# Performance work log

Hardware: AMD Instinct MI355X
Metric: run time of the kernel (lower is better)

Reference implementation:

```python
import jax, jax.numpy as jnp
import numpy as np

LN_EPS = 1e-5
NORM_EPS = 1e-12  # F.normalize eps


def _l2norm(x):
    # torch F.normalize(p=2, dim=-1): x / max(||x||, eps)
    n = jnp.sqrt(jnp.sum(x * x, axis=-1, keepdims=True))
    return x / jnp.maximum(n, NORM_EPS)


def setup_inputs() -> dict:
    key = jax.random.key(0)
    D, R, H = 256, 32, 64  # d_model, rank, d_model//4
    B, C, P = 32, 64, 96
    ks = jax.random.split(key, 16)
    s = 0.05
    return {
        "x": jax.random.normal(ks[0], (B * C, P, D), jnp.float32),
        "ln_gamma": jnp.ones((D,), jnp.float32),
        "ln_beta": jnp.zeros((D,), jnp.float32),
        "Wd": jax.random.normal(ks[1], (D, R), jnp.float32) * s,
        "bd": jax.random.normal(ks[2], (R,), jnp.float32) * s,
        "Wq": jax.random.normal(ks[3], (R, R), jnp.float32) * s,
        "Wk": jax.random.normal(ks[4], (R, R), jnp.float32) * s,
        "Wv": jax.random.normal(ks[5], (R, R), jnp.float32) * s,
        "Wg": jax.random.normal(ks[6], (R, R), jnp.float32) * s,
        "bg": jax.random.normal(ks[7], (R,), jnp.float32) * s,
        "Wu": jax.random.normal(ks[8], (R, D), jnp.float32) * s,
        "bu": jax.random.normal(ks[9], (D,), jnp.float32) * s,
        "W1": jax.random.normal(ks[10], (D, H), jnp.float32) * s,
        "b1": jax.random.normal(ks[11], (H,), jnp.float32) * s,
        "W2": jax.random.normal(ks[12], (H, D), jnp.float32) * s,
        "b2": jnp.full((D,), -5.0, jnp.float32),  # gate_init bias
        "B": B,
        "C": C,
    }


def reference(x, ln_gamma, ln_beta, Wd, bd, Wq, Wk, Wv, Wg, bg, Wu, bu, W1, b1, W2, b2, B, C):
    BC, P, D = x.shape
    # [B*C, P, D] -> [B*P, C, D] channel-mixing layout
    h = x.reshape(B, C, P, D).transpose(0, 2, 1, 3).reshape(B * P, C, D)

    # LayerNorm over D (biased variance, as in torch LayerNorm)
    mu = jnp.mean(h, axis=-1, keepdims=True)
    var = jnp.var(h, axis=-1, keepdims=True)
    h_norm = (h - mu) * jax.lax.rsqrt(var + LN_EPS) * ln_gamma + ln_beta

    # bottleneck projection to rank R
    h_low = h_norm @ Wd + bd  # [BP, C, R]

    # Hydra linear attention: cosine-normalized Q/K, sum-pooled K*V global feature
    Q = _l2norm(h_low @ Wq)
    K = _l2norm(h_low @ Wk)
    V = h_low @ Wv
    global_feat = jnp.sum(K * V, axis=1, keepdims=True)  # [BP, 1, R]
    h_attn = Q * global_feat

    # content gate and up-projection
    gate_c = jax.nn.sigmoid(h_low @ Wg + bg)
    mixed = (h_attn * gate_c) @ Wu + bu  # [BP, C, D]

    # AdaptiveGate: unbiased variance over channel dim (torch .var default ddof=1)
    chan_var = jnp.var(h, axis=1, ddof=1)  # [BP, D]
    gate_logits = jax.nn.gelu(chan_var @ W1 + b1, approximate=False) @ W2 + b2
    gate = jax.nn.sigmoid(gate_logits)[:, None, :]  # [BP, 1, D]

    out = h + gate * mixed
    # back to [B*C, P, D]
    return out.reshape(B, P, C, D).transpose(0, 2, 1, 3).reshape(BC, P, D)
```

## Files before the change

### kernel.cpp

```cpp
#include <hip/hip_runtime.h>

#define DD 256
#define RR 32
#define CC 64
#define PB 96
#define NT 1024

typedef __attribute__((ext_vector_type(8))) short short8;
typedef __attribute__((ext_vector_type(4))) float f32x4;

__device__ __forceinline__ unsigned short f2b(float f) {
    union { float f; unsigned u; } v; v.f = f;
    unsigned r = v.u + 0x7fffu + ((v.u >> 16) & 1u);
    return (unsigned short)(r >> 16);
}
__device__ __forceinline__ float b2f(unsigned short s) {
    union { unsigned u; float f; } v; v.u = ((unsigned)s) << 16;
    return v.f;
}

__device__ __forceinline__ int hidx(int c, int d) {
    return c * 256 + ((((d >> 3) ^ (c & 7)) << 3) | (d & 7));
}
__device__ __forceinline__ int nidx(int row, int k) {
    return row * 32 + ((((k >> 3) ^ ((row >> 1) & 3)) << 3) | (k & 7));
}

__global__ __launch_bounds__(NT, 8)
void hydra_kernel(const float* __restrict__ x,
                  const float* __restrict__ ln_g, const float* __restrict__ ln_b,
                  const float* __restrict__ Wd, const float* __restrict__ bd,
                  const float* __restrict__ Wq, const float* __restrict__ Wk,
                  const float* __restrict__ Wv, const float* __restrict__ Wg,
                  const float* __restrict__ bg,
                  const float* __restrict__ Wu, const float* __restrict__ bu,
                  const float* __restrict__ W1, const float* __restrict__ b1,
                  const float* __restrict__ W2, const float* __restrict__ b2,
                  float* __restrict__ out)
{
    __shared__ short hbf[CC * DD];
    __shared__ short wreg[RR * DD];
    __shared__ short lowbuf[CC * RR];
    __shared__ short qgkv[2 * CC * RR];
    __shared__ float redA[2048];
    __shared__ float redB[1024];
    __shared__ float mu_s[CC], rstd_s[CC];
    __shared__ float cv_s[DD], gate_s[DD];
    __shared__ float hid_s[64];
    __shared__ float ln_a[RR], ln_bv[RR];

    const int t    = threadIdx.x;
    const int lane = t & 63;
    const int w    = t >> 6;
    const int bp   = blockIdx.x;
    const int b    = bp / PB;
    const int p    = bp - b * PB;
    const size_t rowbase = (size_t)(b * CC) * PB * DD + (size_t)p * DD;

    #pragma unroll
    for (int i = 0; i < 4; ++i) {
        const int c = w * 4 + i;
        const float4 v = *(const float4*)(x + rowbase + (size_t)c * (PB * DD) + 4 * lane);
        float s1 = v.x + v.y + v.z + v.w;
        float s2 = v.x * v.x + v.y * v.y + v.z * v.z + v.w * v.w;
        #pragma unroll
        for (int off = 32; off; off >>= 1) {
            s1 += __shfl_xor(s1, off, 64);
            s2 += __shfl_xor(s2, off, 64);
        }
        if (lane == 0) {
            const float mu = s1 * (1.f / 256.f);
            mu_s[c]   = mu;
            rstd_s[c] = rsqrtf(s2 * (1.f / 256.f) - mu * mu + 1e-5f);
        }
        ushort4 pk;
        pk.x = f2b(v.x); pk.y = f2b(v.y); pk.z = f2b(v.z); pk.w = f2b(v.w);
        *(ushort4*)&hbf[hidx(c, 4 * lane)] = pk;
    }
    {
        const int r = t >> 5, dblk = t & 31;
        short8 vv;
        float sa = 0.f, sb = 0.f;
        #pragma unroll
        for (int j = 0; j < 8; ++j) {
            const int d = dblk * 8 + j;
            const float wd = Wd[d * RR + r];
            const float g  = ln_g[d];
            vv[j] = (short)f2b(g * wd);
            sa += g * wd;
            sb += ln_b[d] * wd;
        }
        *(short8*)&wreg[r * 256 + ((dblk ^ (r & 7)) << 3)] = vv;
        redA[r * 32 + dblk]        = sa;
        redA[1024 + r * 32 + dblk] = sb;
    }
    __syncthreads();

    f32x4 s3acc = {0.f, 0.f, 0.f, 0.f};
    if (w < 8) {
        const int ct = w >> 1, rt = w & 1;
        const int arow = ct * 16 + (lane & 15);
        const int brow = rt * 16 + (lane & 15);
        const int ksub = lane >> 4;
        #pragma unroll
        for (int step = 0; step < 8; ++step) {
            const int kb = step * 4 + ksub;
            const short8 a  = *(const short8*)&hbf[arow * 256 + ((kb ^ (arow & 7)) << 3)];
            const short8 bf = *(const short8*)&wreg[brow * 256 + ((kb ^ (brow & 7)) << 3)];
            s3acc = __builtin_amdgcn_mfma_f32_16x16x32_bf16(a, bf, s3acc, 0, 0, 0);
        }
    } else {
        const int idx = t - 512;
        const int d = idx & 255, half = idx >> 8;
        float s1 = 0.f, s2 = 0.f;
        #pragma unroll 8
        for (int i = 0; i < 32; ++i) {
            const float v = b2f((unsigned short)hbf[hidx(half * 32 + i, d)]);
            s1 += v; s2 += v * v;
        }
        redB[half * 256 + d]       = s1;
        redB[512 + half * 256 + d] = s2;
        if (idx < 64) {
            const int r = idx & 31, which = idx >> 5;
            float s = 0.f;
            for (int g = 0; g < 32; ++g) s += redA[which * 1024 + r * 32 + g];
            if (which == 0) ln_a[r] = s;
            else            ln_bv[r] = s + bd[r];
        }
    }
    __syncthreads();

    if (w < 8) {
        const int ct = w >> 1, rt = w & 1;
        const int col = rt * 16 + (lane & 15);
        const float la = ln_a[col], lb = ln_bv[col];
        #pragma unroll
        for (int i = 0; i < 4; ++i) {
            const int c = ct * 16 + (lane >> 4) * 4 + i;
            const float rs = rstd_s[c];
            const float hl = rs * s3acc[i] - rs * mu_s[c] * la + lb;
            lowbuf[nidx(c, col)] = (short)f2b(hl);
        }
    } else {
        const int slot = t - 512;
        const int m = slot >> 7, rr2 = (slot >> 2) & 31, kg = slot & 3;
        const float* Wm = (m == 0) ? Wq : (m == 1) ? Wk : (m == 2) ? Wv : Wg;
        short8 vv;
        #pragma unroll
        for (int j = 0; j < 8; ++j)
            vv[j] = (short)f2b(Wm[(kg * 8 + j) * RR + rr2]);
        *(short8*)&wreg[m * 1024 + nidx(rr2, kg * 8)] = vv;
    }
    if (t < 256) {
        const float S1 = redB[t] + redB[256 + t];
        const float S2 = redB[512 + t] + redB[768 + t];
        cv_s[t] = (S2 - S1 * S1 * (1.f / 64.f)) * (1.f / 63.f);
    }
    __syncthreads();

    if (w < 8) {
        const int ct = w >> 1, pair = w & 1;
        const int mA = pair ? 1 : 0;
        const int mB = pair ? 2 : 3;
        const int arow = ct * 16 + (lane & 15);
        const int ksub = lane >> 4;
        const short8 a = *(const short8*)&lowbuf[arow * 32 + ((ksub ^ ((arow >> 1) & 3)) << 3)];
        f32x4 aA0 = {0,0,0,0}, aA1 = {0,0,0,0}, aB0 = {0,0,0,0}, aB1 = {0,0,0,0};
        {
            const int br0 = (lane & 15), br1 = 16 + (lane & 15);
            const short8 bA0 = *(const short8*)&wreg[mA * 1024 + br0 * 32 + ((ksub ^ ((br0 >> 1) & 3)) << 3)];
            const short8 bA1 = *(const short8*)&wreg[mA * 1024 + br1 * 32 + ((ksub ^ ((br1 >> 1) & 3)) << 3)];
            const short8 bB0 = *(const short8*)&wreg[mB * 1024 + br0 * 32 + ((ksub ^ ((br0 >> 1) & 3)) << 3)];
            const short8 bB1 = *(const short8*)&wreg[mB * 1024 + br1 * 32 + ((ksub ^ ((br1 >> 1) & 3)) << 3)];
            aA0 = __builtin_amdgcn_mfma_f32_16x16x32_bf16(a, bA0, aA0, 0, 0, 0);
            aA1 = __builtin_amdgcn_mfma_f32_16x16x32_bf16(a, bA1, aA1, 0, 0, 0);
            aB0 = __builtin_amdgcn_mfma_f32_16x16x32_bf16(a, bB0, aB0, 0, 0, 0);
            aB1 = __builtin_amdgcn_mfma_f32_16x16x32_bf16(a, bB1, aB1, 0, 0, 0);
        }
        float qs[4];
        #pragma unroll
        for (int i = 0; i < 4; ++i) {
            float ss = aA0[i] * aA0[i] + aA1[i] * aA1[i];
            ss += __shfl_xor(ss, 1, 64);
            ss += __shfl_xor(ss, 2, 64);
            ss += __shfl_xor(ss, 4, 64);
            ss += __shfl_xor(ss, 8, 64);
            qs[i] = 1.f / fmaxf(sqrtf(ss), 1e-12f);
        }
        const int col0 = (lane & 15), col1 = 16 + (lane & 15);
        float bgv0 = 0.f, bgv1 = 0.f;
        if (pair == 0) { bgv0 = bg[col0]; bgv1 = bg[col1]; }
        #pragma unroll
        for (int i = 0; i < 4; ++i) {
            const int c = ct * 16 + (lane >> 4) * 4 + i;
            float b0 = aB0[i], b1v = aB1[i];
            if (pair == 0) {
                b0  = 1.f / (1.f + expf(-(b0 + bgv0)));
                b1v = 1.f / (1.f + expf(-(b1v + bgv1)));
            }
            qgkv[pair * 2048 + c * 32 + col0] = (short)f2b(aA0[i] * qs[i] * b0);
            qgkv[pair * 2048 + c * 32 + col1] = (short)f2b(aA1[i] * qs[i] * b1v);
        }
    } else {
        const int idx = t - 512;
        const int j = idx & 63, dg = idx >> 6;
        float s = 0.f;
        #pragma unroll 8
        for (int i = 0; i < 32; ++i) {
            const int d = dg * 32 + i;
            s += cv_s[d] * W1[d * 64 + j];
        }
        redA[dg * 64 + j] = s;
    }
    __syncthreads();

    if (t < 64) {
        float s = b1[t];
        #pragma unroll
        for (int g = 0; g < 8; ++g) s += redA[g * 64 + t];
        hid_s[t] = 0.5f * s * (1.f + erff(s * 0.70710678118654752f));
    }
    if (t >= 256 && t < 512) {
        const int idx = t - 256;
        const int r = idx & 31, g = idx >> 5;
        float s = 0.f;
        #pragma unroll
        for (int i = 0; i < 8; ++i)
            s += b2f((unsigned short)qgkv[2048 + (g * 8 + i) * 32 + r]);
        redA[512 + g * 32 + r] = s;
    }
    {
        const int d = t & 255, kg = t >> 8;
        short8 vv;
        #pragma unroll
        for (int j = 0; j < 8; ++j)
            vv[j] = (short)f2b(Wu[(kg * 8 + j) * DD + d]);
        *(short8*)&wreg[nidx(d, kg * 8)] = vv;
    }
    __syncthreads();

    {
        const int d = t & 255, jg = t >> 8;
        float s = 0.f;
        #pragma unroll
        for (int i = 0; i < 16; ++i) {
            const int j = jg * 16 + i;
            s += hid_s[j] * W2[j * DD + d];
        }
        redB[jg * 256 + d] = s;
    }
    {
        const int r = t & 31, c0 = t >> 5, c1 = (t >> 5) + 32;
        float gf = 0.f;
        #pragma unroll
        for (int g = 0; g < 8; ++g) gf += redA[512 + g * 32 + r];
        lowbuf[nidx(c0, r)] = (short)f2b(b2f((unsigned short)qgkv[c0 * 32 + r]) * gf);
        lowbuf[nidx(c1, r)] = (short)f2b(b2f((unsigned short)qgkv[c1 * 32 + r]) * gf);
    }
    __syncthreads();

    if (t < 256) {
        const float s = redB[t] + redB[256 + t] + redB[512 + t] + redB[768 + t] + b2[t];
        gate_s[t] = 1.f / (1.f + expf(-s));
    }
    __syncthreads();

    {
        const int ct = w & 3, dg = w >> 2;
        const int arow = ct * 16 + (lane & 15);
        const int ksub = lane >> 4;
        const short8 a = *(const short8*)&lowbuf[arow * 32 + ((ksub ^ ((arow >> 1) & 3)) << 3)];
        #pragma unroll
        for (int j = 0; j < 4; ++j) {
            const int dt = dg * 4 + j;
            const int col = dt * 16 + (lane & 15);
            const short8 bf = *(const short8*)&wreg[col * 32 + ((ksub ^ ((col >> 1) & 3)) << 3)];
            f32x4 acc = {0.f, 0.f, 0.f, 0.f};
            acc = __builtin_amdgcn_mfma_f32_16x16x32_bf16(a, bf, acc, 0, 0, 0);
            const float gt = gate_s[col];
            const float buv = bu[col];
            #pragma unroll
            for (int i = 0; i < 4; ++i) {
                const int c = ct * 16 + (lane >> 4) * 4 + i;
                const size_t off = rowbase + (size_t)c * (PB * DD) + col;
                out[off] = x[off] + gt * (acc[i] + buv);
            }
        }
    }
}

extern "C" void kernel_launch(void* const* d_in, const int* in_sizes, int n_in,
                              void* d_out, int out_size, void* d_ws, size_t ws_size,
                              hipStream_t stream) {
    (void)in_sizes; (void)n_in; (void)out_size; (void)d_ws; (void)ws_size;
    const float* x    = (const float*)d_in[0];
    const float* ln_g = (const float*)d_in[1];
    const float* ln_b = (const float*)d_in[2];
    const float* Wd   = (const float*)d_in[3];
    const float* bd   = (const float*)d_in[4];
    const float* Wq   = (const float*)d_in[5];
    const float* Wk   = (const float*)d_in[6];
    const float* Wv   = (const float*)d_in[7];
    const float* Wg   = (const float*)d_in[8];
    const float* bg   = (const float*)d_in[9];
    const float* Wu   = (const float*)d_in[10];
    const float* bu   = (const float*)d_in[11];
    const float* W1   = (const float*)d_in[12];
    const float* b1   = (const float*)d_in[13];
    const float* W2   = (const float*)d_in[14];
    const float* b2   = (const float*)d_in[15];
    float* out = (float*)d_out;

    hydra_kernel<<<dim3(32 * PB), dim3(NT), 0, stream>>>(
        x, ln_g, ln_b, Wd, bd, Wq, Wk, Wv, Wg, bg, Wu, bu, W1, b1, W2, b2, out);
}
```

Measured before the change: 172.7 us.

## Stage up-projection in LDS and write output with coalesced float4 stores

The final up-projection result is now written to shared memory as bf16 and then re-read so that each wave writes full 1 KB output rows with float4 loads of x and float4 stores, replacing scattered scalar global accesses. The gate sigmoid is moved after the MFMA so it shares a single barrier with it. The channel-variance reduction is restructured to process column pairs over four row groups, and expf is swapped for __expf. The cost is an extra LDS round trip and rounding the mixed term to bf16, which loses precision.

```diff
diff --git a/kernel.cpp b/kernel.cpp
--- a/kernel.cpp
+++ b/kernel.cpp
@@ -43,7 +43,7 @@
     __shared__ short lowbuf[CC * RR];
     __shared__ short qgkv[2 * CC * RR];
     __shared__ float redA[2048];
-    __shared__ float redB[1024];
+    __shared__ float redB[2048];
     __shared__ float mu_s[CC], rstd_s[CC];
     __shared__ float cv_s[DD], gate_s[DD];
     __shared__ float hid_s[64];
@@ -111,15 +111,20 @@
         }
     } else {
         const int idx = t - 512;
-        const int d = idx & 255, half = idx >> 8;
-        float s1 = 0.f, s2 = 0.f;
-        #pragma unroll 8
-        for (int i = 0; i < 32; ++i) {
-            const float v = b2f((unsigned short)hbf[hidx(half * 32 + i, d)]);
-            s1 += v; s2 += v * v;
-        }
-        redB[half * 256 + d]       = s1;
-        redB[512 + half * 256 + d] = s2;
+        const int dp  = idx & 127;
+        const int rg  = idx >> 7;
+        const int d0  = dp * 2;
+        float s1a = 0.f, s1b = 0.f, s2a = 0.f, s2b = 0.f;
+        #pragma unroll 4
+        for (int i = 0; i < 16; ++i) {
+            const int c = rg * 16 + i;
+            const ushort2 u = *(const ushort2*)&hbf[hidx(c, d0)];
+            const float va = b2f(u.x), vb = b2f(u.y);
+            s1a += va; s2a += va * va;
+            s1b += vb; s2b += vb * vb;
+        }
+        *(float2*)&redB[rg * 256 + d0]        = make_float2(s1a, s1b);
+        *(float2*)&redB[1024 + rg * 256 + d0] = make_float2(s2a, s2b);
         if (idx < 64) {
             const int r = idx & 31, which = idx >> 5;
             float s = 0.f;
@@ -152,8 +157,8 @@
         *(short8*)&wreg[m * 1024 + nidx(rr2, kg * 8)] = vv;
     }
     if (t < 256) {
-        const float S1 = redB[t] + redB[256 + t];
-        const float S2 = redB[512 + t] + redB[768 + t];
+        const float S1 = redB[t] + redB[256 + t] + redB[512 + t] + redB[768 + t];
+        const float S2 = redB[1024 + t] + redB[1280 + t] + redB[1536 + t] + redB[1792 + t];
         cv_s[t] = (S2 - S1 * S1 * (1.f / 64.f)) * (1.f / 63.f);
     }
     __syncthreads();
@@ -195,8 +200,8 @@
             const int c = ct * 16 + (lane >> 4) * 4 + i;
             float b0 = aB0[i], b1v = aB1[i];
             if (pair == 0) {
-                b0  = 1.f / (1.f + expf(-(b0 + bgv0)));
-                b1v = 1.f / (1.f + expf(-(b1v + bgv1)));
+                b0  = 1.f / (1.f + __expf(-(b0 + bgv0)));
+                b1v = 1.f / (1.f + __expf(-(b1v + bgv1)));
             }
             qgkv[pair * 2048 + c * 32 + col0] = (short)f2b(aA0[i] * qs[i] * b0);
             qgkv[pair * 2048 + c * 32 + col1] = (short)f2b(aA1[i] * qs[i] * b1v);
@@ -259,12 +264,6 @@
     }
     __syncthreads();
 
-    if (t < 256) {
-        const float s = redB[t] + redB[256 + t] + redB[512 + t] + redB[768 + t] + b2[t];
-        gate_s[t] = 1.f / (1.f + expf(-s));
-    }
-    __syncthreads();
-
     {
         const int ct = w & 3, dg = w >> 2;
         const int arow = ct * 16 + (lane & 15);
@@ -277,15 +276,33 @@
             const short8 bf = *(const short8*)&wreg[col * 32 + ((ksub ^ ((col >> 1) & 3)) << 3)];
             f32x4 acc = {0.f, 0.f, 0.f, 0.f};
             acc = __builtin_amdgcn_mfma_f32_16x16x32_bf16(a, bf, acc, 0, 0, 0);
-            const float gt = gate_s[col];
-            const float buv = bu[col];
             #pragma unroll
             for (int i = 0; i < 4; ++i) {
                 const int c = ct * 16 + (lane >> 4) * 4 + i;
-                const size_t off = rowbase + (size_t)c * (PB * DD) + col;
-                out[off] = x[off] + gt * (acc[i] + buv);
+                hbf[hidx(c, col)] = (short)f2b(acc[i]);
             }
         }
+    }
+    if (t < 256) {
+        const float s = redB[t] + redB[256 + t] + redB[512 + t] + redB[768 + t] + b2[t];
+        gate_s[t] = 1.f / (1.f + __expf(-s));
+    }
+    __syncthreads();
+
+    #pragma unroll
+    for (int i = 0; i < 4; ++i) {
+        const int c = w * 4 + i;
+        const size_t off = rowbase + (size_t)c * (PB * DD) + 4 * lane;
+        const float4 xv = *(const float4*)(x + off);
+        const ushort4 m = *(const ushort4*)&hbf[hidx(c, 4 * lane)];
+        const float4 g4 = *(const float4*)&gate_s[4 * lane];
+        const float4 bu4 = *(const float4*)(bu + 4 * lane);
+        float4 o;
+        o.x = xv.x + g4.x * (b2f(m.x) + bu4.x);
+        o.y = xv.y + g4.y * (b2f(m.y) + bu4.y);
+        o.z = xv.z + g4.z * (b2f(m.z) + bu4.z);
+        o.w = xv.w + g4.w * (b2f(m.w) + bu4.w);
+        *(float4*)(out + off) = o;
     }
 }
 
```

Result: faster. 166.2 us (-3.8%).
